# Kernel tuning notes

Measured on AMD Instinct MI355X. Metric: run time of the kernel, lower is better.

## Reference

```python
import jax, jax.numpy as jnp
import numpy as np

B, N, D, OUT = 4, 4096, 2048, 2048
E, RANK, TOP_K = 8, 16, 2
ALPHA = 16.0
SCALING = ALPHA / RANK


def setup_inputs() -> dict:
    key = jax.random.key(0)
    k1, k2, k3, k4 = jax.random.split(key, 4)
    x = jax.random.normal(k1, (B, N, D), dtype=jnp.float32)
    weight = jax.random.normal(k2, (OUT, D), dtype=jnp.float32) * (1.0 / np.sqrt(D))
    router_w = jax.random.normal(k3, (E, D), dtype=jnp.float32) * 0.02
    experts_A = jax.random.normal(k4, (E, D, RANK), dtype=jnp.float32) * (1.0 / np.sqrt(RANK))
    # experts_B is zero-initialized in the module; use small random values so the
    # LoRA branch contributes non-trivially to the output for kernel testing.
    experts_B = jax.random.normal(jax.random.fold_in(key, 5), (E, RANK, OUT), dtype=jnp.float32) * 0.02
    return {"x": x, "weight": weight, "router_w": router_w,
            "experts_A": experts_A, "experts_B": experts_B}


def reference(x, weight, router_w, experts_A, experts_B):
    # base = F.linear(x, weight)  (no bias)
    base = jnp.einsum('bnd,od->bno', x, weight)
    # router logits: x @ W_r^T -> (B, N, E)
    logits = jnp.einsum('bnd,ed->bne', x, router_w)
    # top-k sparse routing: keep top-k logits, set rest to -inf, softmax
    topk_vals, topk_idx = jax.lax.top_k(logits, TOP_K)  # (B,N,K)
    keep = jax.nn.one_hot(topk_idx, E, dtype=jnp.bool_).any(axis=-2)  # (B,N,E)
    masked = jnp.where(keep, logits, -jnp.inf)
    router_weights = jax.nn.softmax(masked, axis=-1)  # (B,N,E)
    # per-expert low-rank down/up projection, weighted by router
    lora_down = jnp.einsum('bnd,edr->bner', x, experts_A)  # (B,N,E,rank)
    weighted = lora_down * router_weights[..., None]
    moe_out = jnp.einsum('bner,erd->bnd', weighted, experts_B)  # (B,N,OUT)
    return base + SCALING * moe_out
```

## Files before the change

kernel.cpp:

```cpp
#include <hip/hip_runtime.h>
#include <stdint.h>

#define D_DIM 2048
#define OUT_DIM 2048
#define NTOK 16384
#define SCALING 1.0f
#define NT_TILES 34

typedef unsigned short u16;
typedef __attribute__((ext_vector_type(8))) short s16x8;
typedef __attribute__((ext_vector_type(4))) float f32x4;

#define WZ_OFF  0u
#define AZ_OFF  8388608u
#define BZ_OFF  8912896u
#define CZ_OFF  9437184u
#define W8_OFF  13631488u
#define XB_OFF  14155776u
#define WS_BIG   81264640u

__device__ inline u16 f2bf(float f) {
  union { float f; uint32_t u; } v; v.f = f;
  uint32_t u = v.u;
  u += 0x7FFFu + ((u >> 16) & 1u);
  return (u16)(u >> 16);
}

__global__ __launch_bounds__(256) void k_prep_router(
    const float* __restrict__ W, const float* __restrict__ A,
    const float* __restrict__ Bf, const float* __restrict__ x,
    const float* __restrict__ rw,
    u16* __restrict__ Wz, u16* __restrict__ Az, u16* __restrict__ Bz,
    float* __restrict__ w8, u16* __restrict__ xb) {
  int bid = blockIdx.x;
  if (bid < 4096) {
    int idx = bid * 256 + threadIdx.x;
    int o  = idx >> 9;
    int k0 = (idx & 511) * 4;
    const float4 v = *(const float4*)&W[(size_t)o * D_DIM + k0];
    int s = (o & 7) << 3;
    int dst = (k0 & ~63) | ((k0 & 63) ^ s);
    uint32_t p0 = (uint32_t)f2bf(v.x) | ((uint32_t)f2bf(v.y) << 16);
    uint32_t p1 = (uint32_t)f2bf(v.z) | ((uint32_t)f2bf(v.w) << 16);
    *(uint2*)&Wz[(size_t)o * D_DIM + dst] = make_uint2(p0, p1);
    return;
  }
  if (bid < 5120) {
    int idx = (bid - 4096) * 256 + threadIdx.x;
    float v = A[idx];
    int r = idx & 15;
    int d = (idx >> 4) & 2047;
    int e = idx >> 15;
    int er = e * 16 + r;
    int s = (er & 7) << 3;
    int dst = (d & ~63) | ((d & 63) ^ s);
    Az[(size_t)er * D_DIM + dst] = f2bf(v);
    return;
  }
  if (bid < 6144) {
    int idx = (bid - 5120) * 256 + threadIdx.x;
    float v = Bf[idx];
    int er = idx >> 11;
    int o  = idx & 2047;
    int s = (o & 7) << 3;
    int dst = (er & 64) | ((er & 63) ^ s);
    Bz[(size_t)o * 128 + dst] = f2bf(v);
    return;
  }
  int lane = threadIdx.x & 63, wid = threadIdx.x >> 6;
  int t = (bid - 6144) * 4 + wid;
  const float* xr = x + (size_t)t * D_DIM;
  float4 xv[8];
#pragma unroll
  for (int j = 0; j < 8; ++j) xv[j] = *(const float4*)&xr[j * 256 + lane * 4];
  int s = (t & 7) << 3;
#pragma unroll
  for (int j = 0; j < 8; ++j) {
    int c4 = j * 256 + lane * 4;
    int dst = (c4 & ~63) | ((c4 & 63) ^ s);
    uint32_t p0 = (uint32_t)f2bf(xv[j].x) | ((uint32_t)f2bf(xv[j].y) << 16);
    uint32_t p1 = (uint32_t)f2bf(xv[j].z) | ((uint32_t)f2bf(xv[j].w) << 16);
    *(uint2*)&xb[(size_t)t * D_DIM + dst] = make_uint2(p0, p1);
  }
  float lg[8];
#pragma unroll
  for (int e = 0; e < 8; ++e) {
    float a = 0.f;
#pragma unroll
    for (int j = 0; j < 8; ++j) {
      float4 rv = *(const float4*)&rw[e * D_DIM + j * 256 + lane * 4];
      a = fmaf(xv[j].x, rv.x, a); a = fmaf(xv[j].y, rv.y, a);
      a = fmaf(xv[j].z, rv.z, a); a = fmaf(xv[j].w, rv.w, a);
    }
#pragma unroll
    for (int off = 32; off; off >>= 1) a += __shfl_xor(a, off, 64);
    lg[e] = a;
  }
  int i0 = 0;
#pragma unroll
  for (int e = 1; e < 8; ++e) if (lg[e] > lg[i0]) i0 = e;
  int i1 = (i0 == 0) ? 1 : 0;
#pragma unroll
  for (int e = 0; e < 8; ++e) if (e != i0 && lg[e] > lg[i1]) i1 = e;
  float e1 = expf(lg[i1] - lg[i0]);
  float inv = 1.f / (1.f + e1);
  float w0 = inv * SCALING, w1 = e1 * inv * SCALING;
  if (lane < 8)
    w8[(size_t)t * 8 + lane] = (lane == i0) ? w0 : (lane == i1) ? w1 : 0.f;
}

__global__ __launch_bounds__(256) void k_lora64(const u16* __restrict__ xb,
                                                const u16* __restrict__ Az,
                                                const float* __restrict__ w8,
                                                u16* __restrict__ Cz) {
  __shared__ u16 Alds[2][64 * 64];
  __shared__ u16 Blds[2][128 * 64];
  __shared__ float w8s[64 * 8];
  int tid = threadIdx.x, lane = tid & 63, wid = tid >> 6;
  int t0 = blockIdx.x * 64;
  w8s[tid] = w8[(size_t)t0 * 8 + tid];
  w8s[256 + tid] = w8[(size_t)t0 * 8 + 256 + tid];
  f32x4 acc[8];
#pragma unroll
  for (int n = 0; n < 8; ++n) acc[n] = (f32x4){0.f, 0.f, 0.f, 0.f};
  const int ce = (lane >> 4) * 8;

  auto stage = [&](int kc, int buf) {
    if (kc > 31) kc = 31;
#pragma unroll
    for (int i = 0; i < 2; ++i) {
      const u16* g = xb + (size_t)(t0 + i * 32 + (tid >> 3)) * D_DIM + kc * 64 + (tid & 7) * 8;
      __builtin_amdgcn_global_load_lds(
          (const __attribute__((address_space(1))) void*)g,
          (__attribute__((address_space(3))) void*)(&Alds[buf][0] + i * 2048 + tid * 8), 16, 0, 0);
    }
#pragma unroll
    for (int i = 0; i < 4; ++i) {
      const u16* g = Az + (size_t)(i * 32 + (tid >> 3)) * D_DIM + kc * 64 + (tid & 7) * 8;
      __builtin_amdgcn_global_load_lds(
          (const __attribute__((address_space(1))) void*)g,
          (__attribute__((address_space(3))) void*)(&Blds[buf][0] + i * 2048 + tid * 8), 16, 0, 0);
    }
  };

  stage(0, 0);
  asm volatile("s_waitcnt vmcnt(0)" ::: "memory");
  __builtin_amdgcn_s_barrier();
  for (int kc = 0; kc < 32; ++kc) {
    int cur = kc & 1;
    stage(kc + 1, cur ^ 1);
#pragma unroll
    for (int kk = 0; kk < 2; ++kk) {
      int ar = wid * 16 + (lane & 15);
      s16x8 af = *(const s16x8*)&Alds[cur][ar * 64 + ((ce + kk * 32) ^ ((ar & 7) << 3))];
#pragma unroll
      for (int nf = 0; nf < 8; ++nf) {
        int br = nf * 16 + (lane & 15);
        s16x8 bf = *(const s16x8*)&Blds[cur][br * 64 + ((ce + kk * 32) ^ ((br & 7) << 3))];
        acc[nf] = __builtin_amdgcn_mfma_f32_16x16x32_bf16(af, bf, acc[nf], 0, 0, 0);
      }
    }
    asm volatile("s_waitcnt vmcnt(0)" ::: "memory");
    __builtin_amdgcn_s_barrier();
  }
#pragma unroll
  for (int q = 0; q < 4; ++q) {
    int rloc = wid * 16 + (lane >> 4) * 4 + q;
#pragma unroll
    for (int nf = 0; nf < 8; ++nf) {
      int er = nf * 16 + (lane & 15);
      float v = acc[nf][q] * w8s[rloc * 8 + (er >> 4)];
      int dst = (er & 64) | ((er & 63) ^ ((rloc & 7) << 3));
      Cz[(size_t)(t0 + rloc) * 128 + dst] = f2bf(v);
    }
  }
}

__device__ inline void stg(int kt, int h, int t0, int o0,
                           const u16* __restrict__ xb, const u16* __restrict__ Wz,
                           const u16* __restrict__ Cz, const u16* __restrict__ Bz,
                           u16* AshP, u16* BshP, int tid) {
  if (kt >= NT_TILES) kt = NT_TILES - 1;
  int p = kt & 1;
  const u16* src; int ld; size_t r0; int c0; u16* dst;
  if (h < 2) {
    if (kt < 32) { src = xb; ld = D_DIM; c0 = kt * 64; }
    else         { src = Cz; ld = 128;   c0 = (kt - 32) * 64; }
    r0 = (size_t)t0 + h * 128;
    dst = AshP + p * 16384 + h * 8192;
  } else {
    if (kt < 32) { src = Wz; ld = D_DIM; c0 = kt * 64; }
    else         { src = Bz; ld = 128;   c0 = (kt - 32) * 64; }
    r0 = (size_t)o0 + (h - 2) * 128;
    dst = BshP + p * 16384 + (h - 2) * 8192;
  }
#pragma unroll
  for (int i = 0; i < 2; ++i) {
    const u16* g = src + (r0 + i * 64 + (tid >> 3)) * (size_t)ld + c0 + (tid & 7) * 8;
    __builtin_amdgcn_global_load_lds(
        (const __attribute__((address_space(1))) void*)g,
        (__attribute__((address_space(3))) void*)(dst + i * 4096 + tid * 8), 16, 0, 0);
  }
}

__device__ inline void read_af(const u16* buf, int rbase, int ce, s16x8 a[4][2]) {
#pragma unroll
  for (int i = 0; i < 4; ++i)
#pragma unroll
    for (int kk = 0; kk < 2; ++kk) {
      int r = rbase + i * 16;
      a[i][kk] = *(const s16x8*)&buf[r * 64 + ((ce + kk * 32) ^ ((r & 7) << 3))];
    }
}

__device__ inline void read_b2(const u16* buf, int rbase, int ce, s16x8 b[4][2], int h) {
#pragma unroll
  for (int i = 0; i < 2; ++i)
#pragma unroll
    for (int kk = 0; kk < 2; ++kk) {
      int r = rbase + (h * 2 + i) * 16;
      b[h * 2 + i][kk] = *(const s16x8*)&buf[r * 64 + ((ce + kk * 32) ^ ((r & 7) << 3))];
    }
}

template <int MFH, int NFH>
__device__ inline void mfma_quad(f32x4 acc[8][4], const s16x8 a[4][2],
                                 const s16x8 b[4][2]) {
#pragma unroll
  for (int i = 0; i < 4; ++i)
#pragma unroll
    for (int j = 0; j < 2; ++j)
#pragma unroll
      for (int kk = 0; kk < 2; ++kk)
        acc[MFH * 4 + i][NFH * 2 + j] = __builtin_amdgcn_mfma_f32_16x16x32_bf16(
            a[i][kk], b[NFH * 2 + j][kk], acc[MFH * 4 + i][NFH * 2 + j], 0, 0, 0);
}

__global__ __launch_bounds__(512, 2) void k_main8(const u16* __restrict__ xb,
                                                  const u16* __restrict__ Wz,
                                                  const u16* __restrict__ Cz,
                                                  const u16* __restrict__ Bz,
                                                  float* __restrict__ out) {
  __shared__ u16 Ash[2][16384];
  __shared__ u16 Bsh[2][16384];
  const int tid = threadIdx.x, lane = tid & 63;
  const int wid = tid >> 6, wm = wid >> 2, wn = wid & 3;
  int bid = blockIdx.x;
  int swz = (bid & 7) * 64 + (bid >> 3);
  int mt = swz >> 3, nt = swz & 7;
  int t0 = mt * 256, o0 = nt * 256;
  const int ce = (lane >> 4) * 8;
  const int arb = wm * 128 + (lane & 15);
  const int brb = wn * 64 + (lane & 15);
  u16* A0 = &Ash[0][0];
  u16* B0 = &Bsh[0][0];

  f32x4 acc[8][4];
#pragma unroll
  for (int m = 0; m < 8; ++m)
#pragma unroll
    for (int n = 0; n < 4; ++n) acc[m][n] = (f32x4){0.f, 0.f, 0.f, 0.f};
  s16x8 a[4][2], b[4][2];

  stg(0, 0, t0, o0, xb, Wz, Cz, Bz, A0, B0, tid);
  stg(0, 1, t0, o0, xb, Wz, Cz, Bz, A0, B0, tid);
  stg(0, 2, t0, o0, xb, Wz, Cz, Bz, A0, B0, tid);
  stg(0, 3, t0, o0, xb, Wz, Cz, Bz, A0, B0, tid);
  stg(1, 0, t0, o0, xb, Wz, Cz, Bz, A0, B0, tid);
  stg(1, 1, t0, o0, xb, Wz, Cz, Bz, A0, B0, tid);
  stg(1, 2, t0, o0, xb, Wz, Cz, Bz, A0, B0, tid);
  asm volatile("s_waitcnt vmcnt(6)" ::: "memory");
  __builtin_amdgcn_s_barrier();
  __builtin_amdgcn_sched_barrier(0);
  read_af(&Ash[0][0], arb, ce, a);
  read_b2(&Bsh[0][0], brb, ce, b, 0);

  for (int kt = 0; kt < NT_TILES; ++kt) {
    const int p = kt & 1;
    const u16* Abuf = &Ash[p][0];
    const u16* Bbuf = &Bsh[p][0];
    asm volatile("s_waitcnt lgkmcnt(0)" ::: "memory");
    __builtin_amdgcn_sched_barrier(0);
    __builtin_amdgcn_s_setprio(1);
    mfma_quad<0, 0>(acc, a, b);
    __builtin_amdgcn_s_setprio(0);
    read_b2(Bbuf, brb, ce, b, 1);
    stg(kt + 1, 3, t0, o0, xb, Wz, Cz, Bz, A0, B0, tid);
    __builtin_amdgcn_s_barrier();
    __builtin_amdgcn_sched_barrier(0);
    asm volatile("s_waitcnt lgkmcnt(0)" ::: "memory");
    __builtin_amdgcn_sched_barrier(0);
    __builtin_amdgcn_s_setprio(1);
    mfma_quad<0, 1>(acc, a, b);
    __builtin_amdgcn_s_setprio(0);
    read_af(Abuf, arb + 64, ce, a);
    __builtin_amdgcn_s_barrier();
    __builtin_amdgcn_sched_barrier(0);
    asm volatile("s_waitcnt lgkmcnt(0)" ::: "memory");
    __builtin_amdgcn_sched_barrier(0);
    __builtin_amdgcn_s_setprio(1);
    mfma_quad<1, 0>(acc, a, b);
    __builtin_amdgcn_s_setprio(0);
    stg(kt + 2, 0, t0, o0, xb, Wz, Cz, Bz, A0, B0, tid);
    stg(kt + 2, 1, t0, o0, xb, Wz, Cz, Bz, A0, B0, tid);
    stg(kt + 2, 2, t0, o0, xb, Wz, Cz, Bz, A0, B0, tid);
    asm volatile("s_waitcnt vmcnt(6)" ::: "memory");
    __builtin_amdgcn_s_barrier();
    __builtin_amdgcn_sched_barrier(0);
    __builtin_amdgcn_s_setprio(1);
    mfma_quad<1, 1>(acc, a, b);
    __builtin_amdgcn_s_setprio(0);
    read_af(&Ash[p ^ 1][0], arb, ce, a);
    read_b2(&Bsh[p ^ 1][0], brb, ce, b, 0);
    __builtin_amdgcn_s_barrier();
    __builtin_amdgcn_sched_barrier(0);
  }
  asm volatile("s_waitcnt vmcnt(0) lgkmcnt(0)" ::: "memory");

#pragma unroll
  for (int mf = 0; mf < 8; ++mf)
#pragma unroll
    for (int q = 0; q < 4; ++q) {
      int row = t0 + wm * 128 + mf * 16 + (lane >> 4) * 4 + q;
#pragma unroll
      for (int nf = 0; nf < 4; ++nf) {
        int col = o0 + wn * 64 + nf * 16 + (lane & 15);
        out[(size_t)row * OUT_DIM + col] = acc[mf][nf][q];
      }
    }
}

extern "C" void kernel_launch(void* const* d_in, const int* in_sizes, int n_in,
                              void* d_out, int out_size, void* d_ws, size_t ws_size,
                              hipStream_t stream) {
  const float* x  = (const float*)d_in[0];
  const float* W  = (const float*)d_in[1];
  const float* rw = (const float*)d_in[2];
  const float* eA = (const float*)d_in[3];
  const float* eB = (const float*)d_in[4];
  float* out = (float*)d_out;
  char* ws = (char*)d_ws;
  if (ws_size < WS_BIG) return;

  u16*   Wz = (u16*)(ws + WZ_OFF);
  u16*   Az = (u16*)(ws + AZ_OFF);
  u16*   Bz = (u16*)(ws + BZ_OFF);
  u16*   Cz = (u16*)(ws + CZ_OFF);
  float* w8 = (float*)(ws + W8_OFF);
  u16*   xb = (u16*)(ws + XB_OFF);

  k_prep_router<<<10240, 256, 0, stream>>>(W, eA, eB, x, rw, Wz, Az, Bz, w8, xb);
  k_lora64<<<256, 256, 0, stream>>>(xb, Az, w8, Cz);
  k_main8<<<512, 512, 0, stream>>>(xb, Wz, Cz, Bz, out);
}
```

Before: 250.8 us.

## Unroll main GEMM loop by two and reorder staging against LDS reads

The k-loop is unrolled by two so each half uses fixed LDS buffer pointers. Global-to-LDS staging calls are redistributed and reordered across the four MFMA phases, and LDS reads are issued before the barrier with partial lgkmcnt waits, so that memory traffic overlaps compute more evenly. This adds more barriers per phase and risks hazards in the staging order, which changes which chunks are in flight at each barrier.

Measured after the change: 251.3 us. Within noise of the previous version (+0.2%).

```diff
diff --git a/kernel.cpp b/kernel.cpp
--- a/kernel.cpp
+++ b/kernel.cpp
@@ -236,6 +236,13 @@
             a[i][kk], b[NFH * 2 + j][kk], acc[MFH * 4 + i][NFH * 2 + j], 0, 0, 0);
 }
 
+#define PH_PRE  do { __builtin_amdgcn_s_barrier(); \
+                     asm volatile("s_waitcnt lgkmcnt(0)" ::: "memory"); \
+                     __builtin_amdgcn_sched_barrier(0); \
+                     __builtin_amdgcn_s_setprio(1); } while (0)
+#define PH_POST do { __builtin_amdgcn_s_setprio(0); \
+                     __builtin_amdgcn_s_barrier(); } while (0)
+
 __global__ __launch_bounds__(512, 2) void k_main8(const u16* __restrict__ xb,
                                                   const u16* __restrict__ Wz,
                                                   const u16* __restrict__ Cz,
@@ -252,8 +259,12 @@
   const int ce = (lane >> 4) * 8;
   const int arb = wm * 128 + (lane & 15);
   const int brb = wn * 64 + (lane & 15);
-  u16* A0 = &Ash[0][0];
-  u16* B0 = &Bsh[0][0];
+  u16* A0p = &Ash[0][0];
+  u16* B0p = &Bsh[0][0];
+  const u16* Ab0 = &Ash[0][0];
+  const u16* Bb0 = &Bsh[0][0];
+  const u16* Ab1 = &Ash[0][0] + 16384;
+  const u16* Bb1 = &Bsh[0][0] + 16384;
 
   f32x4 acc[8][4];
 #pragma unroll
@@ -262,60 +273,52 @@
     for (int n = 0; n < 4; ++n) acc[m][n] = (f32x4){0.f, 0.f, 0.f, 0.f};
   s16x8 a[4][2], b[4][2];
 
-  stg(0, 0, t0, o0, xb, Wz, Cz, Bz, A0, B0, tid);
-  stg(0, 1, t0, o0, xb, Wz, Cz, Bz, A0, B0, tid);
-  stg(0, 2, t0, o0, xb, Wz, Cz, Bz, A0, B0, tid);
-  stg(0, 3, t0, o0, xb, Wz, Cz, Bz, A0, B0, tid);
-  stg(1, 0, t0, o0, xb, Wz, Cz, Bz, A0, B0, tid);
-  stg(1, 1, t0, o0, xb, Wz, Cz, Bz, A0, B0, tid);
-  stg(1, 2, t0, o0, xb, Wz, Cz, Bz, A0, B0, tid);
+#define STG(kt, h) stg(kt, h, t0, o0, xb, Wz, Cz, Bz, A0p, B0p, tid)
+
+  STG(0, 0); STG(0, 1); STG(0, 2); STG(0, 3);
+  STG(1, 2); STG(1, 3); STG(1, 0);
   asm volatile("s_waitcnt vmcnt(6)" ::: "memory");
   __builtin_amdgcn_s_barrier();
-  __builtin_amdgcn_sched_barrier(0);
-  read_af(&Ash[0][0], arb, ce, a);
-  read_b2(&Bsh[0][0], brb, ce, b, 0);
-
-  for (int kt = 0; kt < NT_TILES; ++kt) {
-    const int p = kt & 1;
-    const u16* Abuf = &Ash[p][0];
-    const u16* Bbuf = &Bsh[p][0];
-    asm volatile("s_waitcnt lgkmcnt(0)" ::: "memory");
-    __builtin_amdgcn_sched_barrier(0);
-    __builtin_amdgcn_s_setprio(1);
-    mfma_quad<0, 0>(acc, a, b);
-    __builtin_amdgcn_s_setprio(0);
-    read_b2(Bbuf, brb, ce, b, 1);
-    stg(kt + 1, 3, t0, o0, xb, Wz, Cz, Bz, A0, B0, tid);
-    __builtin_amdgcn_s_barrier();
-    __builtin_amdgcn_sched_barrier(0);
-    asm volatile("s_waitcnt lgkmcnt(0)" ::: "memory");
-    __builtin_amdgcn_sched_barrier(0);
-    __builtin_amdgcn_s_setprio(1);
-    mfma_quad<0, 1>(acc, a, b);
-    __builtin_amdgcn_s_setprio(0);
-    read_af(Abuf, arb + 64, ce, a);
-    __builtin_amdgcn_s_barrier();
-    __builtin_amdgcn_sched_barrier(0);
-    asm volatile("s_waitcnt lgkmcnt(0)" ::: "memory");
-    __builtin_amdgcn_sched_barrier(0);
-    __builtin_amdgcn_s_setprio(1);
-    mfma_quad<1, 0>(acc, a, b);
-    __builtin_amdgcn_s_setprio(0);
-    stg(kt + 2, 0, t0, o0, xb, Wz, Cz, Bz, A0, B0, tid);
-    stg(kt + 2, 1, t0, o0, xb, Wz, Cz, Bz, A0, B0, tid);
-    stg(kt + 2, 2, t0, o0, xb, Wz, Cz, Bz, A0, B0, tid);
+
+  for (int it = 0; it < NT_TILES / 2; ++it) {
+    const int t = it * 2;
+    read_af(Ab0, arb, ce, a);
+    read_b2(Bb0, brb, ce, b, 0);
+    STG(t + 1, 1);
+    asm volatile("s_waitcnt lgkmcnt(8)" ::: "memory");
+    PH_PRE; mfma_quad<0, 0>(acc, a, b); PH_POST;
+    read_b2(Bb0, brb, ce, b, 1);
+    PH_PRE; mfma_quad<0, 1>(acc, a, b); PH_POST;
+    read_af(Ab0, arb + 64, ce, a);
+    STG(t + 2, 2);
+    PH_PRE; mfma_quad<1, 0>(acc, a, b); PH_POST;
+    STG(t + 2, 3);
+    STG(t + 2, 0);
     asm volatile("s_waitcnt vmcnt(6)" ::: "memory");
     __builtin_amdgcn_s_barrier();
-    __builtin_amdgcn_sched_barrier(0);
     __builtin_amdgcn_s_setprio(1);
     mfma_quad<1, 1>(acc, a, b);
-    __builtin_amdgcn_s_setprio(0);
-    read_af(&Ash[p ^ 1][0], arb, ce, a);
-    read_b2(&Bsh[p ^ 1][0], brb, ce, b, 0);
+    PH_POST;
+    read_af(Ab1, arb, ce, a);
+    read_b2(Bb1, brb, ce, b, 0);
+    STG(t + 2, 1);
+    asm volatile("s_waitcnt lgkmcnt(8)" ::: "memory");
+    PH_PRE; mfma_quad<0, 0>(acc, a, b); PH_POST;
+    read_b2(Bb1, brb, ce, b, 1);
+    PH_PRE; mfma_quad<0, 1>(acc, a, b); PH_POST;
+    read_af(Ab1, arb + 64, ce, a);
+    STG(t + 3, 2);
+    PH_PRE; mfma_quad<1, 0>(acc, a, b); PH_POST;
+    STG(t + 3, 3);
+    STG(t + 3, 0);
+    asm volatile("s_waitcnt vmcnt(6)" ::: "memory");
     __builtin_amdgcn_s_barrier();
-    __builtin_amdgcn_sched_barrier(0);
+    __builtin_amdgcn_s_setprio(1);
+    mfma_quad<1, 1>(acc, a, b);
+    PH_POST;
   }
   asm volatile("s_waitcnt vmcnt(0) lgkmcnt(0)" ::: "memory");
+#undef STG
 
 #pragma unroll
   for (int mf = 0; mf < 8; ++mf)
```

## Replace hand-interleaved quad-phase MFMA pipeline with simpler two-half loop

Applied to the files above, without the earlier changes.

Removes the hand-tuned four-phase schedule that interleaved LDS fragment reads, partial global-to-LDS stages, setprio and sched_barriers with MFMA quarters. The new loop reads all A/B fragments for each half tile, issues MFMAs in two halves, then stages a whole k-tile two steps ahead between barriers. This leaves instruction interleaving to the compiler and cuts barrier and waitcnt bookkeeping. In exchange it risks less overlap of LDS reads and global loads with MFMA work. It also reuses the stage-0 buffer while it may still be read, unless the barrier placement fully orders this.

Result: no change. 253.1 us (+0.9%).

```diff
diff --git a/kernel.cpp b/kernel.cpp
--- a/kernel.cpp
+++ b/kernel.cpp
@@ -213,27 +213,27 @@
     }
 }
 
-__device__ inline void read_b2(const u16* buf, int rbase, int ce, s16x8 b[4][2], int h) {
-#pragma unroll
-  for (int i = 0; i < 2; ++i)
+__device__ inline void read_b4(const u16* buf, int rbase, int ce, s16x8 b[4][2]) {
+#pragma unroll
+  for (int i = 0; i < 4; ++i)
 #pragma unroll
     for (int kk = 0; kk < 2; ++kk) {
-      int r = rbase + (h * 2 + i) * 16;
-      b[h * 2 + i][kk] = *(const s16x8*)&buf[r * 64 + ((ce + kk * 32) ^ ((r & 7) << 3))];
-    }
-}
-
-template <int MFH, int NFH>
-__device__ inline void mfma_quad(f32x4 acc[8][4], const s16x8 a[4][2],
+      int r = rbase + i * 16;
+      b[i][kk] = *(const s16x8*)&buf[r * 64 + ((ce + kk * 32) ^ ((r & 7) << 3))];
+    }
+}
+
+template <int MFH>
+__device__ inline void mfma_half(f32x4 acc[8][4], const s16x8 a[4][2],
                                  const s16x8 b[4][2]) {
 #pragma unroll
   for (int i = 0; i < 4; ++i)
 #pragma unroll
-    for (int j = 0; j < 2; ++j)
+    for (int j = 0; j < 4; ++j)
 #pragma unroll
       for (int kk = 0; kk < 2; ++kk)
-        acc[MFH * 4 + i][NFH * 2 + j] = __builtin_amdgcn_mfma_f32_16x16x32_bf16(
-            a[i][kk], b[NFH * 2 + j][kk], acc[MFH * 4 + i][NFH * 2 + j], 0, 0, 0);
+        acc[MFH * 4 + i][j] = __builtin_amdgcn_mfma_f32_16x16x32_bf16(
+            a[i][kk], b[j][kk], acc[MFH * 4 + i][j], 0, 0, 0);
 }
 
 __global__ __launch_bounds__(512, 2) void k_main8(const u16* __restrict__ xb,
@@ -252,8 +252,8 @@
   const int ce = (lane >> 4) * 8;
   const int arb = wm * 128 + (lane & 15);
   const int brb = wn * 64 + (lane & 15);
-  u16* A0 = &Ash[0][0];
-  u16* B0 = &Bsh[0][0];
+  u16* A0p = &Ash[0][0];
+  u16* B0p = &Bsh[0][0];
 
   f32x4 acc[8][4];
 #pragma unroll
@@ -262,60 +262,32 @@
     for (int n = 0; n < 4; ++n) acc[m][n] = (f32x4){0.f, 0.f, 0.f, 0.f};
   s16x8 a[4][2], b[4][2];
 
-  stg(0, 0, t0, o0, xb, Wz, Cz, Bz, A0, B0, tid);
-  stg(0, 1, t0, o0, xb, Wz, Cz, Bz, A0, B0, tid);
-  stg(0, 2, t0, o0, xb, Wz, Cz, Bz, A0, B0, tid);
-  stg(0, 3, t0, o0, xb, Wz, Cz, Bz, A0, B0, tid);
-  stg(1, 0, t0, o0, xb, Wz, Cz, Bz, A0, B0, tid);
-  stg(1, 1, t0, o0, xb, Wz, Cz, Bz, A0, B0, tid);
-  stg(1, 2, t0, o0, xb, Wz, Cz, Bz, A0, B0, tid);
-  asm volatile("s_waitcnt vmcnt(6)" ::: "memory");
+#define STG(kt) do { stg(kt, 0, t0, o0, xb, Wz, Cz, Bz, A0p, B0p, tid); \
+                     stg(kt, 1, t0, o0, xb, Wz, Cz, Bz, A0p, B0p, tid); \
+                     stg(kt, 2, t0, o0, xb, Wz, Cz, Bz, A0p, B0p, tid); \
+                     stg(kt, 3, t0, o0, xb, Wz, Cz, Bz, A0p, B0p, tid); } while (0)
+
+  STG(0);
+  STG(1);
+  asm volatile("s_waitcnt vmcnt(8)" ::: "memory");
   __builtin_amdgcn_s_barrier();
-  __builtin_amdgcn_sched_barrier(0);
-  read_af(&Ash[0][0], arb, ce, a);
-  read_b2(&Bsh[0][0], brb, ce, b, 0);
 
   for (int kt = 0; kt < NT_TILES; ++kt) {
     const int p = kt & 1;
-    const u16* Abuf = &Ash[p][0];
-    const u16* Bbuf = &Bsh[p][0];
-    asm volatile("s_waitcnt lgkmcnt(0)" ::: "memory");
-    __builtin_amdgcn_sched_barrier(0);
-    __builtin_amdgcn_s_setprio(1);
-    mfma_quad<0, 0>(acc, a, b);
-    __builtin_amdgcn_s_setprio(0);
-    read_b2(Bbuf, brb, ce, b, 1);
-    stg(kt + 1, 3, t0, o0, xb, Wz, Cz, Bz, A0, B0, tid);
+    const u16* Abuf = A0p + p * 16384;
+    const u16* Bbuf = B0p + p * 16384;
+    read_af(Abuf, arb, ce, a);
+    read_b4(Bbuf, brb, ce, b);
+    mfma_half<0>(acc, a, b);
+    read_af(Abuf, arb + 64, ce, a);
+    mfma_half<1>(acc, a, b);
     __builtin_amdgcn_s_barrier();
-    __builtin_amdgcn_sched_barrier(0);
-    asm volatile("s_waitcnt lgkmcnt(0)" ::: "memory");
-    __builtin_amdgcn_sched_barrier(0);
-    __builtin_amdgcn_s_setprio(1);
-    mfma_quad<0, 1>(acc, a, b);
-    __builtin_amdgcn_s_setprio(0);
-    read_af(Abuf, arb + 64, ce, a);
+    STG(kt + 2);
+    asm volatile("s_waitcnt vmcnt(8)" ::: "memory");
     __builtin_amdgcn_s_barrier();
-    __builtin_amdgcn_sched_barrier(0);
-    asm volatile("s_waitcnt lgkmcnt(0)" ::: "memory");
-    __builtin_amdgcn_sched_barrier(0);
-    __builtin_amdgcn_s_setprio(1);
-    mfma_quad<1, 0>(acc, a, b);
-    __builtin_amdgcn_s_setprio(0);
-    stg(kt + 2, 0, t0, o0, xb, Wz, Cz, Bz, A0, B0, tid);
-    stg(kt + 2, 1, t0, o0, xb, Wz, Cz, Bz, A0, B0, tid);
-    stg(kt + 2, 2, t0, o0, xb, Wz, Cz, Bz, A0, B0, tid);
-    asm volatile("s_waitcnt vmcnt(6)" ::: "memory");
-    __builtin_amdgcn_s_barrier();
-    __builtin_amdgcn_sched_barrier(0);
-    __builtin_amdgcn_s_setprio(1);
-    mfma_quad<1, 1>(acc, a, b);
-    __builtin_amdgcn_s_setprio(0);
-    read_af(&Ash[p ^ 1][0], arb, ce, a);
-    read_b2(&Bsh[p ^ 1][0], brb, ce, b, 0);
-    __builtin_amdgcn_s_barrier();
-    __builtin_amdgcn_sched_barrier(0);
   }
   asm volatile("s_waitcnt vmcnt(0) lgkmcnt(0)" ::: "memory");
+#undef STG
 
 #pragma unroll
   for (int mf = 0; mf < 8; ++mf)
```
